# Kernel optimization log

Hardware: AMD Instinct MI355X
Metric: run time of the kernel (lower is better)

## Reference

```python
import jax, jax.numpy as jnp
import numpy as np

IN, OUT, N = 4096, 4096, 8192

def setup_inputs() -> dict:
    key = jax.random.key(0)
    k = jax.random.split(key, 7)
    sigma_start = 1.0  # log_sigma init = log(1.0) = 0; we use small randn instead for generality
    return {
        "x": jax.random.normal(k[0], (N, IN), dtype=jnp.float32),
        "mu_weight": jax.random.normal(k[1], (OUT, IN), dtype=jnp.float32) * 0.02,
        "log_sigma_weight": jax.random.normal(k[2], (OUT, IN), dtype=jnp.float32) * 0.1 - 3.0,
        "mu_bias": jax.random.normal(k[3], (OUT,), dtype=jnp.float32) * 0.02,
        "log_sigma_bias": jax.random.normal(k[4], (OUT,), dtype=jnp.float32) * 0.1 - 3.0,
        "eps_w": jax.random.normal(k[5], (OUT, IN), dtype=jnp.float32),
        "eps_b": jax.random.normal(k[6], (OUT,), dtype=jnp.float32),
    }

def reference(x, mu_weight, log_sigma_weight, mu_bias, log_sigma_bias, eps_w, eps_b):
    # Reparameterized Gaussian weight sampling: W = mu + exp(log_sigma) * eps
    weight = mu_weight + jnp.exp(log_sigma_weight) * eps_w        # [OUT, IN]
    bias = mu_bias + jnp.exp(log_sigma_bias) * eps_b              # [OUT]
    # F.linear(x, W, b) = x @ W^T + b
    return jnp.einsum("ni,oi->no", x, weight) + bias               # [N, OUT]
```

## Files before the change

### kernel.cpp

```cpp
#include <hip/hip_runtime.h>
#include <hip/hip_bf16.h>
#include <stdint.h>


constexpr int M    = 8192;
constexpr int K    = 4096;
constexpr int NOUT = 4096;

typedef __bf16 bf16x8 __attribute__((ext_vector_type(8)));
typedef float  f32x4  __attribute__((ext_vector_type(4)));
typedef short  short8 __attribute__((ext_vector_type(8)));

#define DI __device__ __forceinline__

DI void gl_lds16(const void* g, void* l) {
  __builtin_amdgcn_global_load_lds(
      (__attribute__((address_space(1))) void*)(g),
      (__attribute__((address_space(3))) void*)(l),
      16, 0, 0);
}

union BF8 {
  __hip_bfloat16 h[8];
  short8 s;
};

__global__ __launch_bounds__(256) void cast_x_kernel(const float* __restrict__ x,
                                                     short* __restrict__ xb) {
  int i = blockIdx.x * 256 + threadIdx.x;
  const float4* src = (const float4*)x;
  float4 f0 = src[2 * i + 0];
  float4 f1 = src[2 * i + 1];
  BF8 u;
  u.h[0] = __float2bfloat16(f0.x);
  u.h[1] = __float2bfloat16(f0.y);
  u.h[2] = __float2bfloat16(f0.z);
  u.h[3] = __float2bfloat16(f0.w);
  u.h[4] = __float2bfloat16(f1.x);
  u.h[5] = __float2bfloat16(f1.y);
  u.h[6] = __float2bfloat16(f1.z);
  u.h[7] = __float2bfloat16(f1.w);
  ((short8*)xb)[i] = u.s;
}

__global__ __launch_bounds__(256) void w_fuse_kernel(const float* __restrict__ mu,
                                                     const float* __restrict__ ls,
                                                     const float* __restrict__ eps,
                                                     short* __restrict__ wb) {
  int i = blockIdx.x * 256 + threadIdx.x;
  const float4* mu4 = (const float4*)mu;
  const float4* ls4 = (const float4*)ls;
  const float4* ep4 = (const float4*)eps;
  float4 m0 = mu4[2 * i + 0], m1 = mu4[2 * i + 1];
  float4 l0 = ls4[2 * i + 0], l1 = ls4[2 * i + 1];
  float4 e0 = ep4[2 * i + 0], e1 = ep4[2 * i + 1];
  BF8 u;
  u.h[0] = __float2bfloat16(m0.x + __expf(l0.x) * e0.x);
  u.h[1] = __float2bfloat16(m0.y + __expf(l0.y) * e0.y);
  u.h[2] = __float2bfloat16(m0.z + __expf(l0.z) * e0.z);
  u.h[3] = __float2bfloat16(m0.w + __expf(l0.w) * e0.w);
  u.h[4] = __float2bfloat16(m1.x + __expf(l1.x) * e1.x);
  u.h[5] = __float2bfloat16(m1.y + __expf(l1.y) * e1.y);
  u.h[6] = __float2bfloat16(m1.z + __expf(l1.z) * e1.z);
  u.h[7] = __float2bfloat16(m1.w + __expf(l1.w) * e1.w);
  ((short8*)wb)[i] = u.s;
}

__global__ __launch_bounds__(256) void bias_kernel(const float* __restrict__ mu_b,
                                                   const float* __restrict__ ls_b,
                                                   const float* __restrict__ eps_b,
                                                   float* __restrict__ bias) {
  int i = blockIdx.x * 256 + threadIdx.x;
  if (i < NOUT) bias[i] = mu_b[i] + expf(ls_b[i]) * eps_b[i];
}

constexpr int BM = 256, BN = 256, BK = 32;
constexpr int NT = K / BK;

__global__ __launch_bounds__(512, 2) void gemm_bt_kernel(const short* __restrict__ A,
                                                         const short* __restrict__ B,
                                                         const float* __restrict__ bias,
                                                         float* __restrict__ C) {
  __shared__ __align__(16) short Alds[4][BM * BK];
  __shared__ __align__(16) short Blds[4][BN * BK];

  const int tid  = threadIdx.x;
  const int lane = tid & 63;
  const int wave = tid >> 6;
  const int wm   = wave >> 2;
  const int wn   = wave & 3;
  const int mrow = lane & 15;
  const int quad = lane >> 4;

  const int bid = blockIdx.x;
  const int swz = (bid & 7) * 64 + (bid >> 3);
  const int m0  = (swz >> 4) * BM;
  const int n0  = (swz & 15) * BN;

  const int c0 = tid, c1 = 512 + tid;
  const int cb0 = (wave << 6);
  const int cb1 = 512 + (wave << 6);
  const int r0 = c0 >> 2, r1 = c1 >> 2;
  const int sl0 = (c0 & 3) ^ ((r0 >> 1) & 3);
  const int sl1 = (c1 & 3) ^ ((r1 >> 1) & 3);
  const short* gA0 = A + (size_t)(m0 + r0) * K + sl0 * 8;
  const short* gA1 = A + (size_t)(m0 + r1) * K + sl1 * 8;
  const short* gB0 = B + (size_t)(n0 + r0) * K + sl0 * 8;
  const short* gB1 = B + (size_t)(n0 + r1) * K + sl1 * 8;

  const int slot = quad ^ ((mrow >> 1) & 3);
  const int aOff = (wm * 128 + mrow) * 64 + slot * 16;
  const int bOff = (wn * 64 + mrow) * 64 + slot * 16;

  f32x4 acc[8][4] = {};

#define STAGE(tt)                                           \
  do {                                                      \
    const int _b = (tt) & 3;                                \
    const int _k = (tt) * BK;                               \
    gl_lds16(gA0 + _k, (char*)Alds[_b] + cb0 * 16);         \
    gl_lds16(gA1 + _k, (char*)Alds[_b] + cb1 * 16);         \
    gl_lds16(gB0 + _k, (char*)Blds[_b] + cb0 * 16);         \
    gl_lds16(gB1 + _k, (char*)Blds[_b] + cb1 * 16);         \
  } while (0)

#define COMPUTE(tt)                                                              \
  do {                                                                           \
    const char* _Ab = (const char*)Alds[(tt) & 3] + aOff;                        \
    const char* _Bb = (const char*)Blds[(tt) & 3] + bOff;                        \
    bf16x8 a[8], b[4];                                                           \
    _Pragma("unroll") for (int mi = 0; mi < 8; ++mi)                             \
        a[mi] = *(const bf16x8*)(_Ab + mi * 1024);                               \
    _Pragma("unroll") for (int ni = 0; ni < 4; ++ni)                             \
        b[ni] = *(const bf16x8*)(_Bb + ni * 1024);                               \
    __builtin_amdgcn_s_setprio(1);                                               \
    _Pragma("unroll") for (int mi = 0; mi < 8; ++mi)                             \
        _Pragma("unroll") for (int ni = 0; ni < 4; ++ni)                         \
            acc[mi][ni] =                                                        \
                __builtin_amdgcn_mfma_f32_16x16x32_bf16(a[mi], b[ni],            \
                                                        acc[mi][ni], 0, 0, 0);  \
    __builtin_amdgcn_s_setprio(0);                                               \
  } while (0)

  STAGE(0);
  STAGE(1);
  STAGE(2);
  asm volatile("s_waitcnt vmcnt(8)" ::: "memory");
  __builtin_amdgcn_s_barrier();

#pragma unroll 4
  for (int t = 0; t < NT - 3; ++t) {
    STAGE(t + 3);
    COMPUTE(t);
    asm volatile("s_waitcnt vmcnt(8)" ::: "memory");
    __builtin_amdgcn_s_barrier();
  }
  COMPUTE(NT - 3);
  asm volatile("s_waitcnt vmcnt(4)" ::: "memory");
  __builtin_amdgcn_s_barrier();
  COMPUTE(NT - 2);
  asm volatile("s_waitcnt vmcnt(0)" ::: "memory");
  __builtin_amdgcn_s_barrier();
  COMPUTE(NT - 1);

#undef STAGE
#undef COMPUTE

#pragma unroll
  for (int ni = 0; ni < 4; ++ni) {
    const int col  = n0 + wn * 64 + ni * 16 + mrow;
    const float bv = bias[col];
#pragma unroll
    for (int mi = 0; mi < 8; ++mi) {
      const int rowb = m0 + wm * 128 + mi * 16 + quad * 4;
#pragma unroll
      for (int r = 0; r < 4; ++r)
        C[(size_t)(rowb + r) * NOUT + col] = acc[mi][ni][r] + bv;
    }
  }
}

extern "C" void kernel_launch(void* const* d_in, const int* in_sizes, int n_in,
                              void* d_out, int out_size, void* d_ws, size_t ws_size,
                              hipStream_t stream) {
  const float* x    = (const float*)d_in[0];
  const float* mu_w = (const float*)d_in[1];
  const float* ls_w = (const float*)d_in[2];
  const float* mu_b = (const float*)d_in[3];
  const float* ls_b = (const float*)d_in[4];
  const float* ep_w = (const float*)d_in[5];
  const float* ep_b = (const float*)d_in[6];
  float* out = (float*)d_out;

  char* ws = (char*)d_ws;
  short* xb   = (short*)(ws);
  short* wb   = (short*)(ws + (size_t)M * K * 2);
  float* bias = (float*)(ws + (size_t)M * K * 2 + (size_t)NOUT * K * 2);

  cast_x_kernel<<<(M * (size_t)K) / 8 / 256, 256, 0, stream>>>(x, xb);
  w_fuse_kernel<<<((size_t)NOUT * K) / 8 / 256, 256, 0, stream>>>(mu_w, ls_w, ep_w, wb);
  bias_kernel<<<(NOUT + 255) / 256, 256, 0, stream>>>(mu_b, ls_b, ep_b, bias);

  gemm_bt_kernel<<<(M / BM) * (NOUT / BN), 512, 0, stream>>>(xb, wb, bias, out);
}
```

Before: 625.0 us.

## Merge prep kernels into one launch and split GEMM k-step into two barrier phases

```diff
diff --git a/kernel.cpp b/kernel.cpp
--- a/kernel.cpp
+++ b/kernel.cpp
@@ -25,53 +25,54 @@
   short8 s;
 };
 
-__global__ __launch_bounds__(256) void cast_x_kernel(const float* __restrict__ x,
-                                                     short* __restrict__ xb) {
-  int i = blockIdx.x * 256 + threadIdx.x;
-  const float4* src = (const float4*)x;
-  float4 f0 = src[2 * i + 0];
-  float4 f1 = src[2 * i + 1];
-  BF8 u;
-  u.h[0] = __float2bfloat16(f0.x);
-  u.h[1] = __float2bfloat16(f0.y);
-  u.h[2] = __float2bfloat16(f0.z);
-  u.h[3] = __float2bfloat16(f0.w);
-  u.h[4] = __float2bfloat16(f1.x);
-  u.h[5] = __float2bfloat16(f1.y);
-  u.h[6] = __float2bfloat16(f1.z);
-  u.h[7] = __float2bfloat16(f1.w);
-  ((short8*)xb)[i] = u.s;
-}
-
-__global__ __launch_bounds__(256) void w_fuse_kernel(const float* __restrict__ mu,
-                                                     const float* __restrict__ ls,
-                                                     const float* __restrict__ eps,
-                                                     short* __restrict__ wb) {
-  int i = blockIdx.x * 256 + threadIdx.x;
-  const float4* mu4 = (const float4*)mu;
-  const float4* ls4 = (const float4*)ls;
-  const float4* ep4 = (const float4*)eps;
-  float4 m0 = mu4[2 * i + 0], m1 = mu4[2 * i + 1];
-  float4 l0 = ls4[2 * i + 0], l1 = ls4[2 * i + 1];
-  float4 e0 = ep4[2 * i + 0], e1 = ep4[2 * i + 1];
-  BF8 u;
-  u.h[0] = __float2bfloat16(m0.x + __expf(l0.x) * e0.x);
-  u.h[1] = __float2bfloat16(m0.y + __expf(l0.y) * e0.y);
-  u.h[2] = __float2bfloat16(m0.z + __expf(l0.z) * e0.z);
-  u.h[3] = __float2bfloat16(m0.w + __expf(l0.w) * e0.w);
-  u.h[4] = __float2bfloat16(m1.x + __expf(l1.x) * e1.x);
-  u.h[5] = __float2bfloat16(m1.y + __expf(l1.y) * e1.y);
-  u.h[6] = __float2bfloat16(m1.z + __expf(l1.z) * e1.z);
-  u.h[7] = __float2bfloat16(m1.w + __expf(l1.w) * e1.w);
-  ((short8*)wb)[i] = u.s;
-}
-
-__global__ __launch_bounds__(256) void bias_kernel(const float* __restrict__ mu_b,
-                                                   const float* __restrict__ ls_b,
-                                                   const float* __restrict__ eps_b,
-                                                   float* __restrict__ bias) {
-  int i = blockIdx.x * 256 + threadIdx.x;
-  if (i < NOUT) bias[i] = mu_b[i] + expf(ls_b[i]) * eps_b[i];
+constexpr int XBLK = (M * K / 8) / 256;
+constexpr int WBLK = (NOUT * K / 8) / 256;
+constexpr int BBLK = (NOUT + 255) / 256;
+
+__global__ __launch_bounds__(256) void prep_kernel(
+    const float* __restrict__ x, short* __restrict__ xb,
+    const float* __restrict__ mu, const float* __restrict__ ls,
+    const float* __restrict__ eps, short* __restrict__ wb,
+    const float* __restrict__ mu_b, const float* __restrict__ ls_b,
+    const float* __restrict__ eps_b, float* __restrict__ bias) {
+  const int b = blockIdx.x;
+  if (b < XBLK) {
+    int i = b * 256 + threadIdx.x;
+    const float4* src = (const float4*)x;
+    float4 f0 = src[2 * i + 0];
+    float4 f1 = src[2 * i + 1];
+    BF8 u;
+    u.h[0] = __float2bfloat16(f0.x);
+    u.h[1] = __float2bfloat16(f0.y);
+    u.h[2] = __float2bfloat16(f0.z);
+    u.h[3] = __float2bfloat16(f0.w);
+    u.h[4] = __float2bfloat16(f1.x);
+    u.h[5] = __float2bfloat16(f1.y);
+    u.h[6] = __float2bfloat16(f1.z);
+    u.h[7] = __float2bfloat16(f1.w);
+    ((short8*)xb)[i] = u.s;
+  } else if (b < XBLK + WBLK) {
+    int i = (b - XBLK) * 256 + threadIdx.x;
+    const float4* mu4 = (const float4*)mu;
+    const float4* ls4 = (const float4*)ls;
+    const float4* ep4 = (const float4*)eps;
+    float4 m0 = mu4[2 * i + 0], m1 = mu4[2 * i + 1];
+    float4 l0 = ls4[2 * i + 0], l1 = ls4[2 * i + 1];
+    float4 e0 = ep4[2 * i + 0], e1 = ep4[2 * i + 1];
+    BF8 u;
+    u.h[0] = __float2bfloat16(m0.x + __expf(l0.x) * e0.x);
+    u.h[1] = __float2bfloat16(m0.y + __expf(l0.y) * e0.y);
+    u.h[2] = __float2bfloat16(m0.z + __expf(l0.z) * e0.z);
+    u.h[3] = __float2bfloat16(m0.w + __expf(l0.w) * e0.w);
+    u.h[4] = __float2bfloat16(m1.x + __expf(l1.x) * e1.x);
+    u.h[5] = __float2bfloat16(m1.y + __expf(l1.y) * e1.y);
+    u.h[6] = __float2bfloat16(m1.z + __expf(l1.z) * e1.z);
+    u.h[7] = __float2bfloat16(m1.w + __expf(l1.w) * e1.w);
+    ((short8*)wb)[i] = u.s;
+  } else {
+    int i = (b - XBLK - WBLK) * 256 + threadIdx.x;
+    if (i < NOUT) bias[i] = mu_b[i] + expf(ls_b[i]) * eps_b[i];
+  }
 }
 
 constexpr int BM = 256, BN = 256, BK = 32;
@@ -113,6 +114,55 @@
   const int bOff = (wn * 64 + mrow) * 64 + slot * 16;
 
   f32x4 acc[8][4] = {};
+  bf16x8 bfr[4];
+
+#define PH0(tt, DOSTAGE)                                                    \
+  do {                                                                      \
+    const char* _Ab = (const char*)Alds[(tt) & 3] + aOff;                   \
+    const char* _Bb = (const char*)Blds[(tt) & 3] + bOff;                   \
+    bf16x8 afr[4];                                                          \
+    _Pragma("unroll") for (int mi = 0; mi < 4; ++mi)                        \
+        afr[mi] = *(const bf16x8*)(_Ab + mi * 1024);                        \
+    _Pragma("unroll") for (int ni = 0; ni < 4; ++ni)                        \
+        bfr[ni] = *(const bf16x8*)(_Bb + ni * 1024);                        \
+    if (DOSTAGE) {                                                          \
+      const int _b = ((tt) + 3) & 3;                                        \
+      const int _k = ((tt) + 3) * BK;                                       \
+      gl_lds16(gA0 + _k, (char*)Alds[_b] + cb0 * 16);                       \
+      gl_lds16(gB0 + _k, (char*)Blds[_b] + cb0 * 16);                       \
+    }                                                                       \
+    __builtin_amdgcn_s_barrier();                                           \
+    __builtin_amdgcn_s_setprio(1);                                          \
+    _Pragma("unroll") for (int mi = 0; mi < 4; ++mi)                        \
+        _Pragma("unroll") for (int ni = 0; ni < 4; ++ni)                    \
+            acc[mi][ni] = __builtin_amdgcn_mfma_f32_16x16x32_bf16(          \
+                afr[mi], bfr[ni], acc[mi][ni], 0, 0, 0);                    \
+    __builtin_amdgcn_s_setprio(0);                                          \
+    __builtin_amdgcn_s_barrier();                                           \
+  } while (0)
+
+#define PH1(tt, DOSTAGE, VMSTR)                                             \
+  do {                                                                      \
+    const char* _Ab = (const char*)Alds[(tt) & 3] + aOff;                   \
+    bf16x8 afr[4];                                                          \
+    _Pragma("unroll") for (int mi = 0; mi < 4; ++mi)                        \
+        afr[mi] = *(const bf16x8*)(_Ab + (4 + mi) * 1024);                  \
+    if (DOSTAGE) {                                                          \
+      const int _b = ((tt) + 3) & 3;                                        \
+      const int _k = ((tt) + 3) * BK;                                       \
+      gl_lds16(gA1 + _k, (char*)Alds[_b] + cb1 * 16);                       \
+      gl_lds16(gB1 + _k, (char*)Blds[_b] + cb1 * 16);                       \
+    }                                                                       \
+    __builtin_amdgcn_s_barrier();                                           \
+    __builtin_amdgcn_s_setprio(1);                                          \
+    _Pragma("unroll") for (int mi = 0; mi < 4; ++mi)                        \
+        _Pragma("unroll") for (int ni = 0; ni < 4; ++ni)                    \
+            acc[4 + mi][ni] = __builtin_amdgcn_mfma_f32_16x16x32_bf16(      \
+                afr[mi], bfr[ni], acc[4 + mi][ni], 0, 0, 0);                \
+    __builtin_amdgcn_s_setprio(0);                                          \
+    asm volatile("s_waitcnt vmcnt(" VMSTR ")" ::: "memory");                \
+    __builtin_amdgcn_s_barrier();                                           \
+  } while (0)
 
 #define STAGE(tt)                                           \
   do {                                                      \
@@ -124,24 +174,6 @@
     gl_lds16(gB1 + _k, (char*)Blds[_b] + cb1 * 16);         \
   } while (0)
 
-#define COMPUTE(tt)                                                              \
-  do {                                                                           \
-    const char* _Ab = (const char*)Alds[(tt) & 3] + aOff;                        \
-    const char* _Bb = (const char*)Blds[(tt) & 3] + bOff;                        \
-    bf16x8 a[8], b[4];                                                           \
-    _Pragma("unroll") for (int mi = 0; mi < 8; ++mi)                             \
-        a[mi] = *(const bf16x8*)(_Ab + mi * 1024);                               \
-    _Pragma("unroll") for (int ni = 0; ni < 4; ++ni)                             \
-        b[ni] = *(const bf16x8*)(_Bb + ni * 1024);                               \
-    __builtin_amdgcn_s_setprio(1);                                               \
-    _Pragma("unroll") for (int mi = 0; mi < 8; ++mi)                             \
-        _Pragma("unroll") for (int ni = 0; ni < 4; ++ni)                         \
-            acc[mi][ni] =                                                        \
-                __builtin_amdgcn_mfma_f32_16x16x32_bf16(a[mi], b[ni],            \
-                                                        acc[mi][ni], 0, 0, 0);  \
-    __builtin_amdgcn_s_setprio(0);                                               \
-  } while (0)
-
   STAGE(0);
   STAGE(1);
   STAGE(2);
@@ -150,21 +182,19 @@
 
 #pragma unroll 4
   for (int t = 0; t < NT - 3; ++t) {
-    STAGE(t + 3);
-    COMPUTE(t);
-    asm volatile("s_waitcnt vmcnt(8)" ::: "memory");
-    __builtin_amdgcn_s_barrier();
+    PH0(t, 1);
+    PH1(t, 1, "8");
   }
-  COMPUTE(NT - 3);
-  asm volatile("s_waitcnt vmcnt(4)" ::: "memory");
-  __builtin_amdgcn_s_barrier();
-  COMPUTE(NT - 2);
-  asm volatile("s_waitcnt vmcnt(0)" ::: "memory");
-  __builtin_amdgcn_s_barrier();
-  COMPUTE(NT - 1);
-
+  PH0(NT - 3, 0);
+  PH1(NT - 3, 0, "4");
+  PH0(NT - 2, 0);
+  PH1(NT - 2, 0, "0");
+  PH0(NT - 1, 0);
+  PH1(NT - 1, 0, "0");
+
+#undef PH0
+#undef PH1
 #undef STAGE
-#undef COMPUTE
 
 #pragma unroll
   for (int ni = 0; ni < 4; ++ni) {
@@ -197,9 +227,8 @@
   short* wb   = (short*)(ws + (size_t)M * K * 2);
   float* bias = (float*)(ws + (size_t)M * K * 2 + (size_t)NOUT * K * 2);
 
-  cast_x_kernel<<<(M * (size_t)K) / 8 / 256, 256, 0, stream>>>(x, xb);
-  w_fuse_kernel<<<((size_t)NOUT * K) / 8 / 256, 256, 0, stream>>>(mu_w, ls_w, ep_w, wb);
-  bias_kernel<<<(NOUT + 255) / 256, 256, 0, stream>>>(mu_b, ls_b, ep_b, bias);
+  prep_kernel<<<XBLK + WBLK + BBLK, 256, 0, stream>>>(x, xb, mu_w, ls_w, ep_w, wb,
+                                                      mu_b, ls_b, ep_b, bias);
 
   gemm_bt_kernel<<<(M / BM) * (NOUT / BN), 512, 0, stream>>>(xb, wb, bias, out);
 }
```

Result: slower. 640.0 us (+2.4%).
